# Performance work log

Hardware: AMD Instinct MI355X
Metric: run time of the kernel (lower is better)

Reference implementation:

```python
import jax, jax.numpy as jnp
import numpy as np
import math

NUM_HEADS = 8


def setup_inputs() -> dict:
    key = jax.random.key(0)
    ks = jax.random.split(key, 6)
    b, s, e = 4, 2048, 512
    x = jax.random.normal(ks[0], (b, s, e), dtype=jnp.float32)
    # 0/1 adjacency matrix as float (it multiplies the scores in the module)
    adj = jax.random.randint(ks[1], (b, s, s), 0, 2).astype(jnp.float32)
    scale = 0.02
    Wqkv_w = jax.random.normal(ks[2], (3 * e, e), dtype=jnp.float32) * scale
    Wqkv_b = jax.random.normal(ks[3], (3 * e,), dtype=jnp.float32) * scale
    out_w = jax.random.normal(ks[4], (e, e), dtype=jnp.float32) * scale
    out_b = jax.random.normal(ks[5], (e,), dtype=jnp.float32) * scale
    return {"x": x, "adj": adj, "Wqkv_w": Wqkv_w, "Wqkv_b": Wqkv_b,
            "out_w": out_w, "out_b": out_b}


def reference(x, adj, Wqkv_w, Wqkv_b, out_w, out_b):
    b, s, e = x.shape
    h = NUM_HEADS
    d = e // h
    # fused qkv projection: (b, s, 3*e) -> (b, s, 3, h, d)
    qkv = (x @ Wqkv_w.T + Wqkv_b).reshape(b, s, 3, h, d)
    qkv = jnp.transpose(qkv, (2, 0, 3, 1, 4))  # (3, b, h, s, d)
    q, k, v = qkv[0], qkv[1], qkv[2]
    inv_sqrt_d = 1.0 / math.sqrt(d)
    scores = jnp.einsum('bhqd,bhkd->bhqk', q, k) * inv_sqrt_d
    scores = jnp.clip(scores * adj[:, None, :, :], -10000.0, 10000.0)
    attn = jax.nn.softmax(scores, axis=-1)
    out = jnp.einsum('bhqk,bhkd->bhqd', attn, v)
    out = jnp.transpose(out, (0, 2, 1, 3)).reshape(b, s, e)  # (b, s, h*d)
    return out @ out_w.T + out_b
```

## Files before the change

kernel.cpp:

```cpp
#include <hip/hip_runtime.h>


typedef __attribute__((ext_vector_type(8))) short bf16x8;
typedef __attribute__((ext_vector_type(4))) float f32x4;
typedef __attribute__((ext_vector_type(4))) unsigned short ushort4v;
typedef __attribute__((ext_vector_type(4))) _Float16 f16x4;
typedef __attribute__((ext_vector_type(8))) _Float16 f16x8;
typedef __attribute__((ext_vector_type(2))) __fp16 h16x2;

#if __has_builtin(__builtin_amdgcn_exp2f)
#define EXP2F(x) __builtin_amdgcn_exp2f(x)
#else
#define EXP2F(x) exp2f(x)
#endif

#define QSCALE 0.18033688011112042f

__device__ __forceinline__ unsigned short f2bf(float f) {
  unsigned int u = __float_as_uint(f);
  u += 0x7FFFu + ((u >> 16) & 1u);
  return (unsigned short)(u >> 16);
}
__device__ __forceinline__ unsigned short f2h(float f) {
  union { _Float16 h; unsigned short u; } cv;
  cv.h = (_Float16)f;
  return cv.u;
}

__device__ __forceinline__ int sbit(unsigned w, int pos) {
  return ((int)(w << (31 - pos))) >> 31;
}

__device__ __forceinline__ f16x8 pk8(const float* p) {
  union { struct { h16x2 a, b, c, d; } s; f16x8 v; } u;
  u.s.a = __builtin_amdgcn_cvt_pkrtz(p[0], p[1]);
  u.s.b = __builtin_amdgcn_cvt_pkrtz(p[2], p[3]);
  u.s.c = __builtin_amdgcn_cvt_pkrtz(p[4], p[5]);
  u.s.d = __builtin_amdgcn_cvt_pkrtz(p[6], p[7]);
  return u.v;
}

__device__ __forceinline__ f32x4 mfma_pv(f16x8 a, f16x8 b, f32x4 c) {
#if __has_builtin(__builtin_amdgcn_mfma_f32_16x16x32_f16)
  return __builtin_amdgcn_mfma_f32_16x16x32_f16(a, b, c, 0, 0, 0);
#else
  union { f16x8 v; struct { f16x4 lo, hi; } s; } ua, ub;
  ua.v = a; ub.v = b;
  c = __builtin_amdgcn_mfma_f32_16x16x16f16(ua.s.lo, ub.s.lo, c, 0, 0, 0);
  return __builtin_amdgcn_mfma_f32_16x16x16f16(ua.s.hi, ub.s.hi, c, 0, 0, 0);
#endif
}

__global__ __launch_bounds__(256) void prep_k(const float* __restrict__ x,
                                              unsigned short* __restrict__ x_bf,
                                              const float* __restrict__ wqkv,
                                              unsigned short* __restrict__ wqkv_bf,
                                              const float* __restrict__ outw,
                                              unsigned short* __restrict__ outw_bf,
                                              const float* __restrict__ adj,
                                              unsigned long long* __restrict__ abits) {
  const int bid = blockIdx.x;
  if (bid < 5120) {
    const float* in; unsigned short* out; int i;
    if (bid < 4096) { in = x; out = x_bf; i = bid * 256 + threadIdx.x; }
    else if (bid < 4864) { in = wqkv; out = wqkv_bf; i = (bid - 4096) * 256 + threadIdx.x; }
    else { in = outw; out = outw_bf; i = (bid - 4864) * 256 + threadIdx.x; }
    float4 v = ((const float4*)in)[i];
    ushort4v o;
    o[0] = f2bf(v.x); o[1] = f2bf(v.y); o[2] = f2bf(v.z); o[3] = f2bf(v.w);
    ((ushort4v*)out)[i] = o;
  } else {
    const int gw = (bid - 5120) * 4 + (threadIdx.x >> 6);
    const int l = threadIdx.x & 63;
    const int b = gw >> 11, q = gw & 2047;
    const float* row = adj + ((size_t)b * 2048 + q) * 2048;
    unsigned long long* ob = abits + (size_t)b * 65536 + q;
#pragma unroll 4
    for (int kt = 0; kt < 32; ++kt) {
      const float v = row[kt * 64 + l];
      const unsigned long long m = __ballot(v != 0.f);
      if (l == 0) ob[(size_t)kt * 2048] = m;
    }
  }
}

template <int MODE>
__global__ __launch_bounds__(256, 3) void gemm128_k(const unsigned short* __restrict__ A,
                                                    const unsigned short* __restrict__ Bt,
                                                    const float* __restrict__ bias, int Kdim,
                                                    int Ntiles, unsigned short* __restrict__ q_out,
                                                    unsigned short* __restrict__ k_out,
                                                    unsigned short* __restrict__ v_out,
                                                    float* __restrict__ f_out) {
  __shared__ union {
    struct { unsigned short A[2][128][40], B[2][128][40]; } s;
    unsigned short T[64][136];
  } u;

  const int t = threadIdx.x;
  const int lane = t & 63, w = t >> 6, ln = lane & 15, quad = lane >> 4;
  const int xcd = blockIdx.x & 7, loc = blockIdx.x >> 3;
  const int mt = xcd * ((gridDim.x >> 3) / Ntiles) + loc / Ntiles;
  const int nt = loc % Ntiles;
  const int wm = (w >> 1) * 64, wn = (w & 1) * 64;
  const int strow = t >> 2, stcol = (t & 3) * 8;

  const size_t abase = (size_t)(mt * 128 + strow) * Kdim + stcol;
  const size_t bbase = (size_t)(nt * 128 + strow) * Kdim + stcol;

  f32x4 acc[4][4];
#pragma unroll
  for (int i = 0; i < 4; ++i)
#pragma unroll
    for (int j = 0; j < 4; ++j) acc[i][j] = (f32x4){0.f, 0.f, 0.f, 0.f};

  bf16x8 a0 = *(const bf16x8*)(A + abase);
  bf16x8 a1 = *(const bf16x8*)(A + abase + (size_t)64 * Kdim);
  bf16x8 b0 = *(const bf16x8*)(Bt + bbase);
  bf16x8 b1 = *(const bf16x8*)(Bt + bbase + (size_t)64 * Kdim);
  *(bf16x8*)&u.s.A[0][strow][stcol] = a0;
  *(bf16x8*)&u.s.A[0][64 + strow][stcol] = a1;
  *(bf16x8*)&u.s.B[0][strow][stcol] = b0;
  *(bf16x8*)&u.s.B[0][64 + strow][stcol] = b1;
  __syncthreads();

  const int iters = Kdim >> 5;
  for (int it = 0; it < iters; ++it) {
    const int cur = it & 1, nxt = cur ^ 1;

    const int kn = ((it + 1) << 5) & (Kdim - 1);
    a0 = *(const bf16x8*)(A + abase + kn);
    a1 = *(const bf16x8*)(A + abase + (size_t)64 * Kdim + kn);
    b0 = *(const bf16x8*)(Bt + bbase + kn);
    b1 = *(const bf16x8*)(Bt + bbase + (size_t)64 * Kdim + kn);

    bf16x8 bfr[4];
#pragma unroll
    for (int nf = 0; nf < 4; ++nf)
      bfr[nf] = *(const bf16x8*)&u.s.B[cur][wn + nf * 16 + ln][quad * 8];
#pragma unroll
    for (int mf = 0; mf < 4; ++mf) {
      bf16x8 af = *(const bf16x8*)&u.s.A[cur][wm + mf * 16 + ln][quad * 8];
#pragma unroll
      for (int nf = 0; nf < 4; ++nf)
        acc[mf][nf] = __builtin_amdgcn_mfma_f32_16x16x32_bf16(af, bfr[nf], acc[mf][nf], 0, 0, 0);
    }

    if (it + 1 < iters) {
      *(bf16x8*)&u.s.A[nxt][strow][stcol] = a0;
      *(bf16x8*)&u.s.A[nxt][64 + strow][stcol] = a1;
      *(bf16x8*)&u.s.B[nxt][strow][stcol] = b0;
      *(bf16x8*)&u.s.B[nxt][64 + strow][stcol] = b1;
      __syncthreads();
    }
  }

  if (MODE == 0 && nt >= 8) {
    const int bb = mt >> 4, sq0 = (mt & 15) * 128;
#pragma unroll
    for (int half = 0; half < 2; ++half) {
      __syncthreads();
      if ((w & 1) == half) {
#pragma unroll
        for (int nf = 0; nf < 4; ++nf) {
          const float bv = bias[nt * 128 + half * 64 + nf * 16 + ln];
#pragma unroll
          for (int mf = 0; mf < 4; ++mf)
#pragma unroll
            for (int r = 0; r < 4; ++r)
              u.T[nf * 16 + ln][wm + mf * 16 + quad * 4 + r] = f2h(acc[mf][nf][r] + bv);
        }
      }
      __syncthreads();
#pragma unroll
      for (int rep = 0; rep < 4; ++rep) {
        const int row = rep * 16 + (t >> 4), c = t & 15;
        const bf16x8 val = *(const bf16x8*)&u.T[row][c * 8];
        const int hd = (nt - 8) * 128 + half * 64 + row;
        const int hh = hd >> 6, dd = hd & 63;
        *(bf16x8*)(v_out + ((size_t)(bb * 8 + hh) * 64 + dd) * 2048 + sq0 + c * 8) = val;
      }
    }
    return;
  }

#pragma unroll
  for (int mf = 0; mf < 4; ++mf) {
    const int m = mt * 128 + wm + mf * 16 + quad * 4;
#pragma unroll
    for (int nf = 0; nf < 4; ++nf) {
      const int n = nt * 128 + wn + nf * 16 + ln;
      const float bv = bias[n];
      if (MODE == 0) {
        const int hd = n & 511;
        const int hh = hd >> 6, dd = hd & 63;
        const int bb = m >> 11, sq = m & 2047;
        if (n < 512) {
#pragma unroll
          for (int r = 0; r < 4; ++r)
            q_out[((size_t)(bb * 8 + hh) * 2048 + sq + r) * 64 + dd] =
                f2bf((acc[mf][nf][r] + bv) * QSCALE);
        } else {
#pragma unroll
          for (int r = 0; r < 4; ++r)
            k_out[((size_t)(bb * 8 + hh) * 2048 + sq + r) * 64 + dd] = f2bf(acc[mf][nf][r] + bv);
        }
      } else {
#pragma unroll
        for (int r = 0; r < 4; ++r) f_out[(size_t)(m + r) * 512 + n] = acc[mf][nf][r] + bv;
      }
    }
  }
}

__global__ __launch_bounds__(256, 2) void attn_k(const unsigned short* __restrict__ Qg,
                                                 const unsigned short* __restrict__ Kg,
                                                 const unsigned short* __restrict__ Vg,
                                                 const unsigned long long* __restrict__ Mg,
                                                 unsigned short* __restrict__ Og) {
  __shared__ unsigned short K_lds[2][64][76];
  __shared__ unsigned short V_lds[2][64][72];
  __shared__ unsigned long long M_lds[2][128];

  const int t = threadIdx.x;
  const int w = t >> 6, lane = t & 63, ln = lane & 15, quad = lane >> 4;
  const int bh = blockIdx.x & 31, qt = blockIdx.x >> 5, bb = bh >> 3;
  const int sbase = qt * 128;

  const unsigned short* Qp = Qg + (size_t)bh * (2048 * 64);
  const unsigned short* Kp = Kg + (size_t)bh * (2048 * 64);
  const unsigned short* Vp = Vg + (size_t)bh * (64 * 2048);
  const unsigned long long* Mp = Mg + (size_t)bb * 65536 + sbase;

  bf16x8 qf[2][2];
#pragma unroll
  for (int qg = 0; qg < 2; ++qg) {
    const int qrow = sbase + w * 32 + qg * 16 + ln;
    qf[qg][0] = *(const bf16x8*)(Qp + (size_t)qrow * 64 + quad * 8);
    qf[qg][1] = *(const bf16x8*)(Qp + (size_t)qrow * 64 + 32 + quad * 8);
  }

  const _Float16 one_h = (_Float16)((ln == 0) ? 1.0f : 0.0f);
  const f16x8 vf_one = (f16x8){one_h, one_h, one_h, one_h, one_h, one_h, one_h, one_h};

  f32x4 acc_o[2][4];
#pragma unroll
  for (int qg = 0; qg < 2; ++qg)
#pragma unroll
    for (int dg = 0; dg < 4; ++dg) acc_o[qg][dg] = (f32x4){0.f, 0.f, 0.f, 0.f};
  f32x4 acc_1[2] = {(f32x4){0.f, 0.f, 0.f, 0.f}, (f32x4){0.f, 0.f, 0.f, 0.f}};

  const int strow = t >> 2;
  const int stcol = (t & 3) * 16;

  const unsigned short* Kl = Kp + (size_t)strow * 64 + stcol;
  const unsigned short* Vl = Vp + (size_t)strow * 2048 + stcol;

  bf16x8 kr0 = *(const bf16x8*)(Kl);
  bf16x8 kr1 = *(const bf16x8*)(Kl + 8);
  bf16x8 vr0 = *(const bf16x8*)(Vl);
  bf16x8 vr1 = *(const bf16x8*)(Vl + 8);
  unsigned long long mreg = (w < 2) ? Mp[w * 64 + lane] : 0ull;
  *(bf16x8*)&K_lds[0][strow][stcol] = kr0;
  *(bf16x8*)&K_lds[0][strow][stcol + 8] = kr1;
  *(bf16x8*)&V_lds[0][strow][stcol] = vr0;
  *(bf16x8*)&V_lds[0][strow][stcol + 8] = vr1;
  if (w < 2) M_lds[0][w * 64 + lane] = mreg;
  __syncthreads();

  const int mq = w * 32 + ln;
  const int kperm = ((ln >> 2) << 3) + (ln & 3);

  for (int kt = 0; kt < 32; ++kt) {
    const int cur = kt & 1, nxt = cur ^ 1;

    kr0 = *(const bf16x8*)(Kl + (size_t)(kt + 1) * 4096);
    kr1 = *(const bf16x8*)(Kl + (size_t)(kt + 1) * 4096 + 8);
    vr0 = *(const bf16x8*)(Vl + (kt + 1) * 64);
    vr1 = *(const bf16x8*)(Vl + (kt + 1) * 64 + 8);
    mreg = (w < 2) ? Mp[(size_t)(kt + 1) * 2048 + w * 64 + lane] : 0ull;

    f32x4 sc[2][4];
#pragma unroll
    for (int h = 0; h < 2; ++h)
#pragma unroll
      for (int e = 0; e < 2; ++e) {
        const int krow = h * 32 + kperm + e * 4;
        bf16x8 kf0 = *(const bf16x8*)&K_lds[cur][krow][quad * 8];
        bf16x8 kf1 = *(const bf16x8*)&K_lds[cur][krow][32 + quad * 8];
#pragma unroll
        for (int qg = 0; qg < 2; ++qg) {
          f32x4 z = (f32x4){0.f, 0.f, 0.f, 0.f};
          z = __builtin_amdgcn_mfma_f32_16x16x32_bf16(kf0, qf[qg][0], z, 0, 0, 0);
          sc[qg][h * 2 + e] = __builtin_amdgcn_mfma_f32_16x16x32_bf16(kf1, qf[qg][1], z, 0, 0, 0);
        }
      }

    f16x8 vfa[2][4];
#pragma unroll
    for (int h = 0; h < 2; ++h)
#pragma unroll
      for (int dg = 0; dg < 4; ++dg)
        vfa[h][dg] = *(const f16x8*)&V_lds[cur][dg * 16 + ln][h * 32 + quad * 8];

    f16x8 pa[2][2];
#pragma unroll
    for (int qg = 0; qg < 2; ++qg) {
      const unsigned long long m64 = M_lds[cur][mq + qg * 16];
#pragma unroll
      for (int h = 0; h < 2; ++h) {
        const unsigned wrd = (h ? (unsigned)(m64 >> 32) : (unsigned)m64) >> (quad * 8);
        float p[8];
#pragma unroll
        for (int e = 0; e < 2; ++e)
#pragma unroll
          for (int r = 0; r < 4; ++r) {
            const int j = e * 4 + r;
            const int se = sbit(wrd, j);
            const float s = __int_as_float(__float_as_int(sc[qg][h * 2 + e][r]) & se);
            p[j] = EXP2F(s);
          }
        pa[qg][h] = pk8(p);
      }
    }

#pragma unroll
    for (int h = 0; h < 2; ++h)
#pragma unroll
      for (int qg = 0; qg < 2; ++qg) {
#pragma unroll
        for (int dg = 0; dg < 4; ++dg)
          acc_o[qg][dg] = mfma_pv(pa[qg][h], vfa[h][dg], acc_o[qg][dg]);
        acc_1[qg] = mfma_pv(pa[qg][h], vf_one, acc_1[qg]);
      }

    if (kt < 31) {
      *(bf16x8*)&K_lds[nxt][strow][stcol] = kr0;
      *(bf16x8*)&K_lds[nxt][strow][stcol + 8] = kr1;
      *(bf16x8*)&V_lds[nxt][strow][stcol] = vr0;
      *(bf16x8*)&V_lds[nxt][strow][stcol + 8] = vr1;
      if (w < 2) M_lds[nxt][w * 64 + lane] = mreg;
      __syncthreads();
    }
  }

  unsigned short* Op = Og + (size_t)bb * 2048 * 512 + (size_t)(bh & 7) * 64;
#pragma unroll
  for (int qg = 0; qg < 2; ++qg)
#pragma unroll
    for (int r = 0; r < 4; ++r) {
      const float inv = 1.0f / __shfl(acc_1[qg][r], quad * 16);
      const int sq = sbase + w * 32 + qg * 16 + quad * 4 + r;
#pragma unroll
      for (int dg = 0; dg < 4; ++dg)
        Op[(size_t)sq * 512 + dg * 16 + ln] = f2bf(acc_o[qg][dg][r] * inv);
    }
}

extern "C" void kernel_launch(void* const* d_in, const int* in_sizes, int n_in, void* d_out,
                              int out_size, void* d_ws, size_t ws_size, hipStream_t stream) {
  const float* x = (const float*)d_in[0];
  const float* adj = (const float*)d_in[1];
  const float* wqkv = (const float*)d_in[2];
  const float* bqkv = (const float*)d_in[3];
  const float* outw = (const float*)d_in[4];
  const float* outb = (const float*)d_in[5];
  float* out = (float*)d_out;

  char* ws = (char*)d_ws;
  unsigned short* x_bf = (unsigned short*)(ws);
  unsigned short* wqkv_bf = (unsigned short*)(ws + 8388608);
  unsigned short* outw_bf = (unsigned short*)(ws + 9961472);
  unsigned long long* abits = (unsigned long long*)(ws + 10485760);
  unsigned short* Qb = (unsigned short*)(ws + 27262976);
  unsigned short* Kb = (unsigned short*)(ws + 35651584);
  unsigned short* Vb = (unsigned short*)(ws + 44040192);
  unsigned short* Ob = (unsigned short*)(ws + 52428800);

  prep_k<<<7168, 256, 0, stream>>>(x, x_bf, wqkv, wqkv_bf, outw, outw_bf, adj, abits);

  gemm128_k<0><<<768, 256, 0, stream>>>(x_bf, wqkv_bf, bqkv, 512, 12, Qb, Kb, Vb, nullptr);

  attn_k<<<512, 256, 0, stream>>>(Qb, Kb, Vb, abits, Ob);

  gemm128_k<1><<<256, 256, 0, stream>>>(Ob, outw_bf, outb, 512, 4, nullptr, nullptr, nullptr, out);
}
```

Baseline: 215.7 us.

## Load K, V and mask fragments directly from global memory, dropping LDS staging

The attention kernel stops staging K, V and mask tiles through double-buffered shared memory. Each wave now reads its MFMA operand fragments straight from global memory every iteration, which removes the LDS writes, LDS reads and per-iteration __syncthreads. In exchange, every wave loads the same K/V tile redundantly and relies on the L1/L2 caches to absorb that. There is also no software prefetch, so global load latency sits on the critical path of each iteration.

```diff
diff --git a/kernel.cpp b/kernel.cpp
--- a/kernel.cpp
+++ b/kernel.cpp
@@ -218,10 +218,6 @@
                                                  const unsigned short* __restrict__ Vg,
                                                  const unsigned long long* __restrict__ Mg,
                                                  unsigned short* __restrict__ Og) {
-  __shared__ unsigned short K_lds[2][64][76];
-  __shared__ unsigned short V_lds[2][64][72];
-  __shared__ unsigned long long M_lds[2][128];
-
   const int t = threadIdx.x;
   const int w = t >> 6, lane = t & 63, ln = lane & 15, quad = lane >> 4;
   const int bh = blockIdx.x & 31, qt = blockIdx.x >> 5, bb = bh >> 3;
@@ -230,7 +226,6 @@
   const unsigned short* Qp = Qg + (size_t)bh * (2048 * 64);
   const unsigned short* Kp = Kg + (size_t)bh * (2048 * 64);
   const unsigned short* Vp = Vg + (size_t)bh * (64 * 2048);
-  const unsigned long long* Mp = Mg + (size_t)bb * 65536 + sbase;
 
   bf16x8 qf[2][2];
 #pragma unroll
@@ -250,63 +245,59 @@
     for (int dg = 0; dg < 4; ++dg) acc_o[qg][dg] = (f32x4){0.f, 0.f, 0.f, 0.f};
   f32x4 acc_1[2] = {(f32x4){0.f, 0.f, 0.f, 0.f}, (f32x4){0.f, 0.f, 0.f, 0.f}};
 
-  const int strow = t >> 2;
-  const int stcol = (t & 3) * 16;
-
-  const unsigned short* Kl = Kp + (size_t)strow * 64 + stcol;
-  const unsigned short* Vl = Vp + (size_t)strow * 2048 + stcol;
-
-  bf16x8 kr0 = *(const bf16x8*)(Kl);
-  bf16x8 kr1 = *(const bf16x8*)(Kl + 8);
-  bf16x8 vr0 = *(const bf16x8*)(Vl);
-  bf16x8 vr1 = *(const bf16x8*)(Vl + 8);
-  unsigned long long mreg = (w < 2) ? Mp[w * 64 + lane] : 0ull;
-  *(bf16x8*)&K_lds[0][strow][stcol] = kr0;
-  *(bf16x8*)&K_lds[0][strow][stcol + 8] = kr1;
-  *(bf16x8*)&V_lds[0][strow][stcol] = vr0;
-  *(bf16x8*)&V_lds[0][strow][stcol + 8] = vr1;
-  if (w < 2) M_lds[0][w * 64 + lane] = mreg;
-  __syncthreads();
-
-  const int mq = w * 32 + ln;
   const int kperm = ((ln >> 2) << 3) + (ln & 3);
 
+  const unsigned short* kh0 = Kp + (size_t)kperm * 64 + quad * 8;
+  const unsigned short* kh1 = kh0 + 2048;
+  const unsigned short* vb0 = Vp + (size_t)(0 * 16 + ln) * 2048 + quad * 8;
+  const unsigned short* vb1 = Vp + (size_t)(1 * 16 + ln) * 2048 + quad * 8;
+  const unsigned short* vb2 = Vp + (size_t)(2 * 16 + ln) * 2048 + quad * 8;
+  const unsigned long long* mb = Mg + (size_t)bb * 65536 + sbase + w * 32 + ln;
+  const unsigned short* vb3 = Vp + (size_t)(3 * 16 + ln) * 2048 + quad * 8;
+
   for (int kt = 0; kt < 32; ++kt) {
-    const int cur = kt & 1, nxt = cur ^ 1;
-
-    kr0 = *(const bf16x8*)(Kl + (size_t)(kt + 1) * 4096);
-    kr1 = *(const bf16x8*)(Kl + (size_t)(kt + 1) * 4096 + 8);
-    vr0 = *(const bf16x8*)(Vl + (kt + 1) * 64);
-    vr1 = *(const bf16x8*)(Vl + (kt + 1) * 64 + 8);
-    mreg = (w < 2) ? Mp[(size_t)(kt + 1) * 2048 + w * 64 + lane] : 0ull;
+    bf16x8 kf000 = *(const bf16x8*)(kh0);
+    bf16x8 kf001 = *(const bf16x8*)(kh0 + 32);
+    bf16x8 kf010 = *(const bf16x8*)(kh0 + 256);
+    bf16x8 kf011 = *(const bf16x8*)(kh0 + 288);
+    bf16x8 kf100 = *(const bf16x8*)(kh1);
+    bf16x8 kf101 = *(const bf16x8*)(kh1 + 32);
+    bf16x8 kf110 = *(const bf16x8*)(kh1 + 256);
+    bf16x8 kf111 = *(const bf16x8*)(kh1 + 288);
+    const unsigned long long m64_0 = mb[0];
+    const unsigned long long m64_1 = mb[16];
+    f16x8 vfa[2][4];
+    vfa[0][0] = *(const f16x8*)(vb0);
+    vfa[1][0] = *(const f16x8*)(vb0 + 32);
+    vfa[0][1] = *(const f16x8*)(vb1);
+    vfa[1][1] = *(const f16x8*)(vb1 + 32);
+    vfa[0][2] = *(const f16x8*)(vb2);
+    vfa[1][2] = *(const f16x8*)(vb2 + 32);
+    vfa[0][3] = *(const f16x8*)(vb3);
+    vfa[1][3] = *(const f16x8*)(vb3 + 32);
 
     f32x4 sc[2][4];
 #pragma unroll
-    for (int h = 0; h < 2; ++h)
-#pragma unroll
-      for (int e = 0; e < 2; ++e) {
-        const int krow = h * 32 + kperm + e * 4;
-        bf16x8 kf0 = *(const bf16x8*)&K_lds[cur][krow][quad * 8];
-        bf16x8 kf1 = *(const bf16x8*)&K_lds[cur][krow][32 + quad * 8];
-#pragma unroll
-        for (int qg = 0; qg < 2; ++qg) {
-          f32x4 z = (f32x4){0.f, 0.f, 0.f, 0.f};
-          z = __builtin_amdgcn_mfma_f32_16x16x32_bf16(kf0, qf[qg][0], z, 0, 0, 0);
-          sc[qg][h * 2 + e] = __builtin_amdgcn_mfma_f32_16x16x32_bf16(kf1, qf[qg][1], z, 0, 0, 0);
-        }
-      }
-
-    f16x8 vfa[2][4];
-#pragma unroll
-    for (int h = 0; h < 2; ++h)
-#pragma unroll
-      for (int dg = 0; dg < 4; ++dg)
-        vfa[h][dg] = *(const f16x8*)&V_lds[cur][dg * 16 + ln][h * 32 + quad * 8];
+    for (int qg = 0; qg < 2; ++qg) {
+      f32x4 z;
+      z = (f32x4){0.f, 0.f, 0.f, 0.f};
+      z = __builtin_amdgcn_mfma_f32_16x16x32_bf16(kf000, qf[qg][0], z, 0, 0, 0);
+      sc[qg][0] = __builtin_amdgcn_mfma_f32_16x16x32_bf16(kf001, qf[qg][1], z, 0, 0, 0);
+      z = (f32x4){0.f, 0.f, 0.f, 0.f};
+      z = __builtin_amdgcn_mfma_f32_16x16x32_bf16(kf010, qf[qg][0], z, 0, 0, 0);
+      sc[qg][1] = __builtin_amdgcn_mfma_f32_16x16x32_bf16(kf011, qf[qg][1], z, 0, 0, 0);
+      z = (f32x4){0.f, 0.f, 0.f, 0.f};
+      z = __builtin_amdgcn_mfma_f32_16x16x32_bf16(kf100, qf[qg][0], z, 0, 0, 0);
+      sc[qg][2] = __builtin_amdgcn_mfma_f32_16x16x32_bf16(kf101, qf[qg][1], z, 0, 0, 0);
+      z = (f32x4){0.f, 0.f, 0.f, 0.f};
+      z = __builtin_amdgcn_mfma_f32_16x16x32_bf16(kf110, qf[qg][0], z, 0, 0, 0);
+      sc[qg][3] = __builtin_amdgcn_mfma_f32_16x16x32_bf16(kf111, qf[qg][1], z, 0, 0, 0);
+    }
 
     f16x8 pa[2][2];
 #pragma unroll
     for (int qg = 0; qg < 2; ++qg) {
-      const unsigned long long m64 = M_lds[cur][mq + qg * 16];
+      const unsigned long long m64 = qg ? m64_1 : m64_0;
 #pragma unroll
       for (int h = 0; h < 2; ++h) {
         const unsigned wrd = (h ? (unsigned)(m64 >> 32) : (unsigned)m64) >> (quad * 8);
@@ -334,14 +325,9 @@
         acc_1[qg] = mfma_pv(pa[qg][h], vf_one, acc_1[qg]);
       }
 
-    if (kt < 31) {
-      *(bf16x8*)&K_lds[nxt][strow][stcol] = kr0;
-      *(bf16x8*)&K_lds[nxt][strow][stcol + 8] = kr1;
-      *(bf16x8*)&V_lds[nxt][strow][stcol] = vr0;
-      *(bf16x8*)&V_lds[nxt][strow][stcol + 8] = vr1;
-      if (w < 2) M_lds[nxt][w * 64 + lane] = mreg;
-      __syncthreads();
-    }
+    kh0 += 4096; kh1 += 4096;
+    vb0 += 64; vb1 += 64; vb2 += 64; vb3 += 64;
+    mb += 2048;
   }
 
   unsigned short* Op = Og + (size_t)bb * 2048 * 512 + (size_t)(bh & 7) * 64;
```

After: 289.8 us. 34.4% more time.
